# Optimization experiments

Measured on AMD Instinct MI355X. Metric: run time of the kernel, lower is better.

The kernel has to match this reference:

```python
import jax, jax.numpy as jnp
import numpy as np
import math

N = 2048; L = 100; D_IN = 128; D_STATE = 16; D_INNER = 256
MAMBA_DIM = 128; GAT_HID = 64; HEADS = 4; GAT_OUT = 64


def _lin(key, fin, fout, scale=0.02):
    k1, k2 = jax.random.split(key)
    return (jax.random.normal(k1, (fin, fout), jnp.float32) * scale,
            jnp.zeros((fout,), jnp.float32))


def setup_inputs() -> dict:
    key = jax.random.key(0)
    ks = jax.random.split(key, 16)
    temporal_data = jax.random.normal(ks[0], (N, L, D_IN), jnp.float32)
    graph_x = jax.random.normal(ks[1], (N, D_IN), jnp.float32)
    adj = (jax.random.uniform(ks[2], (N, N)) < 0.005).astype(jnp.float32)
    adj_matrix = jnp.maximum(adj, jnp.eye(N, dtype=jnp.float32))
    pos_emb = jax.random.normal(ks[3], (1, 100, D_IN), jnp.float32)
    Wi, bi = _lin(ks[4], D_IN, D_INNER)
    Wg, bg = _lin(ks[5], D_IN, D_INNER)
    A_log = jnp.linspace(math.log(1e-3), math.log(0.1), D_STATE).reshape(1, D_STATE).astype(jnp.float32)
    Wb, bb = _lin(ks[6], D_INNER, D_STATE)
    Wc, bc = _lin(ks[7], D_IN, D_STATE)
    Wo, bo = _lin(ks[8], D_INNER, D_IN)
    Wfc, bfc = _lin(ks[9], D_IN, MAMBA_DIM)
    W1 = jax.random.normal(ks[10], (HEADS, D_IN, GAT_HID), jnp.float32) * 0.05
    a1 = jax.random.normal(ks[11], (HEADS, 2 * GAT_HID), jnp.float32) * 0.05
    W2 = jax.random.normal(ks[12], (1, HEADS * GAT_HID, GAT_OUT), jnp.float32) * 0.05
    a2 = jax.random.normal(ks[13], (1, 2 * GAT_OUT), jnp.float32) * 0.05
    return dict(temporal_data=temporal_data, graph_x=graph_x, adj_matrix=adj_matrix,
                pos_emb=pos_emb, Wi=Wi, bi=bi, Wg=Wg, bg=bg, A_log=A_log,
                Wb=Wb, bb=bb, Wc=Wc, bc=bc, Wo=Wo, bo=bo, Wfc=Wfc, bfc=bfc,
                W1=W1, a1=a1, W2=W2, a2=a2)


def _mamba(x, pos_emb, Wi, bi, Wg, bg, A_log, Wb, bb, Wc, bc, Wo, bo):
    Bt, Ls, _ = x.shape
    x = x + pos_emb[:, :Ls, :]
    x_gated = (x @ Wi + bi) * jax.nn.sigmoid(x @ Wg + bg)   # [B,L,d_inner]
    Bmat = x_gated @ Wb + bb                                 # [B,L,d_state]
    Cmat = x @ Wc + bc                                       # [B,L,d_state]
    A = jnp.exp(0.01 * jnp.exp(A_log))                       # [1,d_state] (dt=0.01)

    def step(h, bc):
        b, c = bc
        h = A * h + b
        return h, h * c

    h0 = jnp.zeros((Bt, A_log.shape[1]), x.dtype)
    _, ys = jax.lax.scan(step, h0, (jnp.swapaxes(Bmat, 0, 1), jnp.swapaxes(Cmat, 0, 1)))
    y = jnp.swapaxes(ys, 0, 1)                               # [B,L,d_state]
    d_inner = Wo.shape[0]
    out_exp = jnp.concatenate(
        [y, jnp.zeros((Bt, Ls, d_inner - y.shape[-1]), x.dtype)], axis=-1)
    return out_exp @ Wo + bo


def _gat_layer(x, adj, W, a, concat):
    # x: [N,Fin], W: [H,Fin,Fout], a: [H,2*Fout]
    F_out = W.shape[2]
    xt = jnp.einsum('nf,hfo->hno', x, W)                     # [H,N,Fout]
    e_src = jnp.einsum('hno,ho->hn', xt, a[:, :F_out])       # a . x_i part
    e_dst = jnp.einsum('hno,ho->hn', xt, a[:, F_out:])       # a . x_j part
    e = jax.nn.leaky_relu(e_src[:, :, None] + e_dst[:, None, :], 0.2)
    e = jnp.where(adj[None, :, :] > 0, e, -jnp.inf)
    att = jax.nn.softmax(e, axis=2)                          # masked entries -> 0
    h_prime = jnp.einsum('hij,hjo->hio', att, xt)            # [H,N,Fout]
    if concat:
        return jnp.transpose(h_prime, (1, 0, 2)).reshape(x.shape[0], -1)
    return h_prime.mean(axis=0)


def reference(temporal_data, graph_x, adj_matrix, pos_emb, Wi, bi, Wg, bg, A_log,
              Wb, bb, Wc, bc, Wo, bo, Wfc, bfc, W1, a1, W2, a2):
    mamba_out = _mamba(temporal_data, pos_emb, Wi, bi, Wg, bg, A_log, Wb, bb, Wc, bc, Wo, bo)
    mamba_features = mamba_out @ Wfc + bfc
    # GAT stack (dropout is identity in eval mode)
    h = _gat_layer(graph_x, adj_matrix, W1, a1, concat=True)
    h = jax.nn.relu(h)
    gat_features = _gat_layer(h, adj_matrix, W2, a2, concat=False)
    return mamba_features, gat_features
```

## Files before the change

kernel.cpp:

```cpp
#include <hip/hip_runtime.h>
#include <hip/hip_bf16.h>

#define N_NODES 2048
#define L_SEQ   100
#define ROWS    (N_NODES * L_SEQ)
#define HEADS   4
#define GHID    64

typedef __attribute__((ext_vector_type(8))) short bf16x8;
typedef __attribute__((ext_vector_type(4))) float floatx4;

__device__ __forceinline__ short f2bf(float f) {
    union { float f; unsigned u; } v; v.f = f;
    return (short)((v.u + 0x8000u) >> 16);
}

constexpr size_t OFF_WCOMB = 0;
constexpr size_t OFF_BCOMB = 2048;
constexpr size_t OFF_AEXP  = 2176;
constexpr size_t OFF_WIGS  = 2192;
constexpr size_t OFF_WBS   = 34960;
constexpr size_t OFF_WCS   = 37008;
constexpr size_t OFF_BM    = 38032;
constexpr size_t OFF_CM    = OFF_BM + (size_t)ROWS * 16;
constexpr size_t OFF_XT1   = OFF_BM;
constexpr size_t OFF_ES1   = OFF_XT1 + (size_t)HEADS * N_NODES * GHID;
constexpr size_t OFF_ED1   = OFF_ES1 + HEADS * N_NODES;
constexpr size_t OFF_H1    = OFF_ED1 + HEADS * N_NODES;
constexpr size_t OFF_XT2   = OFF_H1 + (size_t)N_NODES * 256;
constexpr size_t OFF_ES2   = OFF_XT2 + (size_t)N_NODES * 64;
constexpr size_t OFF_ED2   = OFF_ES2 + N_NODES;

__global__ void k0_comb(const float* __restrict__ Wo, const float* __restrict__ bo,
                        const float* __restrict__ Wfc, const float* __restrict__ bfc,
                        const float* __restrict__ A_log, float* __restrict__ ws) {
    const int b = blockIdx.x, f2 = threadIdx.x;
    if (b < 16) {
        float a = 0.f;
        for (int f = 0; f < 128; f++) a += Wo[b * 128 + f] * Wfc[f * 128 + f2];
        ws[OFF_WCOMB + b * 128 + f2] = a;
    } else {
        float acc = bfc[f2];
        for (int f = 0; f < 128; f++) acc += bo[f] * Wfc[f * 128 + f2];
        ws[OFF_BCOMB + f2] = acc;
        if (f2 < 16) ws[OFF_AEXP + f2] = expf(0.01f * expf(A_log[f2]));
    }
}

__global__ void k0_prep(const float* __restrict__ Wi, const float* __restrict__ Wg,
                        const float* __restrict__ Wb, const float* __restrict__ Wc,
                        float* __restrict__ ws) {
    int i = blockIdx.x * 256 + threadIdx.x;
    short* wigs = (short*)(ws + OFF_WIGS);
    short* wbs  = (short*)(ws + OFF_WBS);
    short* wcs  = (short*)(ws + OFF_WCS);
    if (i < 65536) {
        int j = i & 7, lane = (i >> 3) & 63, ks = (i >> 9) & 3, nt = i >> 11;
        int w = nt >> 3, t = nt & 7;
        int col = w * 64 + (t & 3) * 16 + (lane & 15);
        int k   = ks * 32 + (lane >> 4) * 8 + j;
        float v = (t < 4) ? Wi[k * 256 + col] : Wg[k * 256 + col];
        wigs[i] = f2bf(v);
    } else if (i < 65536 + 4096) {
        int ii = i - 65536;
        int j = ii & 7, lane = (ii >> 3) & 63, ks = ii >> 9;
        int k = ks * 32 + (lane >> 4) * 8 + j, n = lane & 15;
        wbs[ii] = f2bf(Wb[k * 16 + n]);
    } else if (i < 65536 + 4096 + 2048) {
        int ii = i - 65536 - 4096;
        int j = ii & 7, lane = (ii >> 3) & 63, ks = ii >> 9;
        int k = ks * 32 + (lane >> 4) * 8 + j, n = lane & 15;
        wcs[ii] = f2bf(Wc[k * 16 + n]);
    }
}

__global__ __launch_bounds__(256) void k1_mfma(
    const float* __restrict__ temporal, const float* __restrict__ pos,
    const float* __restrict__ bi, const float* __restrict__ bg,
    const float* __restrict__ bb, const float* __restrict__ bc,
    const float* __restrict__ ws, float* __restrict__ Bm, float* __restrict__ Cm) {
    __shared__ short xbf[64][136];
    __shared__ short gbf[64][264];
    const int tid = threadIdx.x, wave = tid >> 6, lane = tid & 63;
    const int m = lane & 15, quad = lane >> 4;
    const int r0 = blockIdx.x * 64;

#pragma unroll
    for (int i = 0; i < 8; i++) {
        int f4  = i * 256 + tid;
        int row = f4 >> 5;
        int c4  = (f4 & 31) * 4;
        int r = r0 + row, l = r % L_SEQ;
        float4 tv = *(const float4*)(temporal + (size_t)r * 128 + c4);
        float4 pv = *(const float4*)(pos + l * 128 + c4);
        short4 sv;
        sv.x = f2bf(tv.x + pv.x); sv.y = f2bf(tv.y + pv.y);
        sv.z = f2bf(tv.z + pv.z); sv.w = f2bf(tv.w + pv.w);
        *(short4*)&xbf[row][c4] = sv;
    }
    __syncthreads();

    const short* Wigs = (const short*)(ws + OFF_WIGS);
    floatx4 acc[4][8] = {};
#pragma unroll
    for (int ks = 0; ks < 4; ks++) {
        bf16x8 bfr[8];
#pragma unroll
        for (int nt = 0; nt < 8; nt++)
            bfr[nt] = *(const bf16x8*)(Wigs + (size_t)(((wave * 8 + nt) * 4 + ks) * 64 + lane) * 8);
        bf16x8 afr[4];
#pragma unroll
        for (int mt = 0; mt < 4; mt++)
            afr[mt] = *(const bf16x8*)&xbf[mt * 16 + m][ks * 32 + quad * 8];
#pragma unroll
        for (int mt = 0; mt < 4; mt++)
#pragma unroll
            for (int nt = 0; nt < 8; nt++)
                acc[mt][nt] = __builtin_amdgcn_mfma_f32_16x16x32_bf16(
                    afr[mt], bfr[nt], acc[mt][nt], 0, 0, 0);
    }

    const float NL2E = -1.44269504f;
#pragma unroll
    for (int tp = 0; tp < 4; tp++) {
        int col = wave * 64 + tp * 16 + m;
        float biv = bi[col];
        float bgs = bg[col] * NL2E;
#pragma unroll
        for (int mt = 0; mt < 4; mt++) {
#pragma unroll
            for (int r = 0; r < 4; r++) {
                float li = acc[mt][tp][r] + biv;
                float ex = __builtin_amdgcn_exp2f(fmaf(acc[mt][tp + 4][r], NL2E, bgs));
                float g  = li * __builtin_amdgcn_rcpf(1.f + ex);
                gbf[mt * 16 + quad * 4 + r][col] = f2bf(g);
            }
        }
    }
    __syncthreads();

    const short* Wbs = (const short*)(ws + OFF_WBS);
    const short* Wcs = (const short*)(ws + OFF_WCS);
    floatx4 accB = {}, accC = {};
#pragma unroll
    for (int ks = 0; ks < 8; ks++) {
        bf16x8 a = *(const bf16x8*)&gbf[wave * 16 + m][ks * 32 + quad * 8];
        bf16x8 b = *(const bf16x8*)(Wbs + (size_t)(ks * 64 + lane) * 8);
        accB = __builtin_amdgcn_mfma_f32_16x16x32_bf16(a, b, accB, 0, 0, 0);
    }
#pragma unroll
    for (int ks = 0; ks < 4; ks++) {
        bf16x8 a = *(const bf16x8*)&xbf[wave * 16 + m][ks * 32 + quad * 8];
        bf16x8 b = *(const bf16x8*)(Wcs + (size_t)(ks * 64 + lane) * 8);
        accC = __builtin_amdgcn_mfma_f32_16x16x32_bf16(a, b, accC, 0, 0, 0);
    }
    float bbv = bb[m], bcv = bc[m];
#pragma unroll
    for (int r = 0; r < 4; r++) {
        int row = r0 + wave * 16 + quad * 4 + r;
        Bm[(size_t)row * 16 + m] = accB[r] + bbv;
        Cm[(size_t)row * 16 + m] = accC[r] + bcv;
    }
}

__global__ __launch_bounds__(128) void k2_scan(const float* __restrict__ ws,
                                               float* __restrict__ out) {
    __shared__ float sb[1600], sc[1600];
    const int n = blockIdx.x, f = threadIdx.x;
    const float4* Bm4 = (const float4*)(ws + OFF_BM + (size_t)n * 1600);
    const float4* Cm4 = (const float4*)(ws + OFF_CM + (size_t)n * 1600);
#pragma unroll
    for (int i = 0; i < 4; i++) {
        int idx = i * 128 + f;
        if (idx < 400) {
            ((float4*)sb)[idx] = Bm4[idx];
            ((float4*)sc)[idx] = Cm4[idx];
        }
    }
    float w[16], A[16], h[16];
#pragma unroll
    for (int s = 0; s < 16; s++) {
        w[s] = ws[OFF_WCOMB + s * 128 + f];
        A[s] = ws[OFF_AEXP + s];
        h[s] = 0.f;
    }
    const float bcb = ws[OFF_BCOMB + f];
    __syncthreads();
    for (int l = 0; l < L_SEQ; l++) {
        float acc = bcb;
#pragma unroll
        for (int s = 0; s < 16; s++) {
            h[s] = A[s] * h[s] + sb[l * 16 + s];
            acc += h[s] * sc[l * 16 + s] * w[s];
        }
        out[((size_t)n * L_SEQ + l) * 128 + f] = acc;
    }
}

__global__ __launch_bounds__(64) void k4_xt1(const float* __restrict__ gx,
                                             const float* __restrict__ W1,
                                             const float* __restrict__ a1,
                                             float* __restrict__ ws) {
    const int b = blockIdx.x;
    const int h = b >> 11;
    const int n = b & 2047;
    const int o = threadIdx.x;
    float acc = 0.f;
    for (int f = 0; f < 128; f++)
        acc += gx[n * 128 + f] * W1[(h * 128 + f) * 64 + o];
    ws[OFF_XT1 + ((size_t)h * 2048 + n) * 64 + o] = acc;
    float es = acc * a1[h * 128 + o];
    float ed = acc * a1[h * 128 + 64 + o];
#pragma unroll
    for (int off = 32; off > 0; off >>= 1) {
        es += __shfl_down(es, off);
        ed += __shfl_down(ed, off);
    }
    if (o == 0) { ws[OFF_ES1 + h * 2048 + n] = es; ws[OFF_ED1 + h * 2048 + n] = ed; }
}

__global__ __launch_bounds__(256) void k5_att1(const float* __restrict__ adj,
                                               const float* __restrict__ ws,
                                               float* __restrict__ h1out) {
    __shared__ int list[2048];
    __shared__ int cnt;
    const int n = blockIdx.x, tid = threadIdx.x;
    if (tid == 0) cnt = 0;
    __syncthreads();
    for (int j = tid; j < 2048; j += 256)
        if (adj[(size_t)n * 2048 + j] > 0.f) list[atomicAdd(&cnt, 1)] = j;
    __syncthreads();
    const int h = tid >> 6, o = tid & 63;
    const float  es = ws[OFF_ES1 + h * 2048 + n];
    const float* ed = ws + OFF_ED1 + h * 2048;
    const float* xt = ws + OFF_XT1 + (size_t)h * 2048 * 64;
    float num = 0.f, den = 0.f;
    const int mm = cnt;
    for (int ii = 0; ii < mm; ii++) {
        int j = list[ii];
        float e = es + ed[j];
        e = (e > 0.f) ? e : 0.2f * e;
        float wgt = expf(e);
        den += wgt;
        num += wgt * xt[(size_t)j * 64 + o];
    }
    float v = num / den;
    h1out[(size_t)n * 256 + h * 64 + o] = v > 0.f ? v : 0.f;
}

__global__ __launch_bounds__(64) void k6_xt2(const float* __restrict__ W2,
                                             const float* __restrict__ a2,
                                             float* __restrict__ ws) {
    const int n = blockIdx.x, o = threadIdx.x;
    const float* h1 = ws + OFF_H1 + (size_t)n * 256;
    float acc = 0.f;
    for (int f = 0; f < 256; f++) acc += h1[f] * W2[f * 64 + o];
    ws[OFF_XT2 + (size_t)n * 64 + o] = acc;
    float es = acc * a2[o];
    float ed = acc * a2[64 + o];
#pragma unroll
    for (int off = 32; off > 0; off >>= 1) {
        es += __shfl_down(es, off);
        ed += __shfl_down(ed, off);
    }
    if (o == 0) { ws[OFF_ES2 + n] = es; ws[OFF_ED2 + n] = ed; }
}

__global__ __launch_bounds__(64) void k7_att2(const float* __restrict__ adj,
                                              const float* __restrict__ ws,
                                              float* __restrict__ gout) {
    __shared__ int list[2048];
    __shared__ int cnt;
    const int n = blockIdx.x, o = threadIdx.x;
    if (o == 0) cnt = 0;
    __syncthreads();
    for (int j = o; j < 2048; j += 64)
        if (adj[(size_t)n * 2048 + j] > 0.f) list[atomicAdd(&cnt, 1)] = j;
    __syncthreads();
    const float es = ws[OFF_ES2 + n];
    float num = 0.f, den = 0.f;
    const int mm = cnt;
    for (int ii = 0; ii < mm; ii++) {
        int j = list[ii];
        float e = es + ws[OFF_ED2 + j];
        e = (e > 0.f) ? e : 0.2f * e;
        float wgt = expf(e);
        den += wgt;
        num += wgt * ws[OFF_XT2 + (size_t)j * 64 + o];
    }
    gout[(size_t)n * 64 + o] = num / den;
}

extern "C" void kernel_launch(void* const* d_in, const int* in_sizes, int n_in,
                              void* d_out, int out_size, void* d_ws, size_t ws_size,
                              hipStream_t stream) {
    const float* temporal = (const float*)d_in[0];
    const float* graph_x  = (const float*)d_in[1];
    const float* adj      = (const float*)d_in[2];
    const float* pos      = (const float*)d_in[3];
    const float* Wi  = (const float*)d_in[4];
    const float* bi  = (const float*)d_in[5];
    const float* Wg  = (const float*)d_in[6];
    const float* bg  = (const float*)d_in[7];
    const float* A_log = (const float*)d_in[8];
    const float* Wb  = (const float*)d_in[9];
    const float* bb  = (const float*)d_in[10];
    const float* Wc  = (const float*)d_in[11];
    const float* bc  = (const float*)d_in[12];
    const float* Wo  = (const float*)d_in[13];
    const float* bo  = (const float*)d_in[14];
    const float* Wfc = (const float*)d_in[15];
    const float* bfc = (const float*)d_in[16];
    const float* W1  = (const float*)d_in[17];
    const float* a1  = (const float*)d_in[18];
    const float* W2  = (const float*)d_in[19];
    const float* a2  = (const float*)d_in[20];

    float* ws = (float*)d_ws;
    float* out_mamba = (float*)d_out;
    float* out_gat   = out_mamba + (size_t)ROWS * 128;

    k0_comb<<<17, 128, 0, stream>>>(Wo, bo, Wfc, bfc, A_log, ws);
    k0_prep<<<280, 256, 0, stream>>>(Wi, Wg, Wb, Wc, ws);
    k1_mfma<<<ROWS / 64, 256, 0, stream>>>(temporal, pos, bi, bg, bb, bc, ws,
                                           ws + OFF_BM, ws + OFF_CM);
    k2_scan<<<N_NODES, 128, 0, stream>>>(ws, out_mamba);
    k4_xt1<<<HEADS * N_NODES, 64, 0, stream>>>(graph_x, W1, a1, ws);
    k5_att1<<<N_NODES, 256, 0, stream>>>(adj, ws, ws + OFF_H1);
    k6_xt2<<<N_NODES, 64, 0, stream>>>(W2, a2, ws);
    k7_att2<<<N_NODES, 64, 0, stream>>>(adj, ws, out_gat);
}
```

Measured before the change: 378.1 us.

## Split k1 work across 8 waves to halve per-wave accumulators

```diff
diff --git a/kernel.cpp b/kernel.cpp
--- a/kernel.cpp
+++ b/kernel.cpp
@@ -74,7 +74,7 @@
     }
 }
 
-__global__ __launch_bounds__(256) void k1_mfma(
+__global__ __launch_bounds__(512, 4) void k1_mfma(
     const float* __restrict__ temporal, const float* __restrict__ pos,
     const float* __restrict__ bi, const float* __restrict__ bg,
     const float* __restrict__ bb, const float* __restrict__ bc,
@@ -84,14 +84,15 @@
     const int tid = threadIdx.x, wave = tid >> 6, lane = tid & 63;
     const int m = lane & 15, quad = lane >> 4;
     const int r0 = blockIdx.x * 64;
-
-#pragma unroll
-    for (int i = 0; i < 8; i++) {
-        int f4  = i * 256 + tid;
+    const int l0 = r0 % L_SEQ;
+
+#pragma unroll
+    for (int i = 0; i < 4; i++) {
+        int f4  = i * 512 + tid;
         int row = f4 >> 5;
         int c4  = (f4 & 31) * 4;
-        int r = r0 + row, l = r % L_SEQ;
-        float4 tv = *(const float4*)(temporal + (size_t)r * 128 + c4);
+        int l = l0 + row; if (l >= L_SEQ) l -= L_SEQ;
+        float4 tv = *(const float4*)(temporal + (size_t)(r0 + row) * 128 + c4);
         float4 pv = *(const float4*)(pos + l * 128 + c4);
         short4 sv;
         sv.x = f2bf(tv.x + pv.x); sv.y = f2bf(tv.y + pv.y);
@@ -101,13 +102,16 @@
     __syncthreads();
 
     const short* Wigs = (const short*)(ws + OFF_WIGS);
-    floatx4 acc[4][8] = {};
+    const int wg = wave >> 1, wp = wave & 1;
+    floatx4 acc[4][4] = {};
 #pragma unroll
     for (int ks = 0; ks < 4; ks++) {
-        bf16x8 bfr[8];
-#pragma unroll
-        for (int nt = 0; nt < 8; nt++)
-            bfr[nt] = *(const bf16x8*)(Wigs + (size_t)(((wave * 8 + nt) * 4 + ks) * 64 + lane) * 8);
+        bf16x8 bfr[4];
+#pragma unroll
+        for (int jl = 0; jl < 4; jl++) {
+            int ntg = wg * 8 + wp * 2 + (jl & 1) + ((jl >> 1) << 2);
+            bfr[jl] = *(const bf16x8*)(Wigs + (size_t)((ntg * 4 + ks) * 64 + lane) * 8);
+        }
         bf16x8 afr[4];
 #pragma unroll
         for (int mt = 0; mt < 4; mt++)
@@ -115,15 +119,15 @@
 #pragma unroll
         for (int mt = 0; mt < 4; mt++)
 #pragma unroll
-            for (int nt = 0; nt < 8; nt++)
-                acc[mt][nt] = __builtin_amdgcn_mfma_f32_16x16x32_bf16(
-                    afr[mt], bfr[nt], acc[mt][nt], 0, 0, 0);
+            for (int jl = 0; jl < 4; jl++)
+                acc[mt][jl] = __builtin_amdgcn_mfma_f32_16x16x32_bf16(
+                    afr[mt], bfr[jl], acc[mt][jl], 0, 0, 0);
     }
 
     const float NL2E = -1.44269504f;
 #pragma unroll
-    for (int tp = 0; tp < 4; tp++) {
-        int col = wave * 64 + tp * 16 + m;
+    for (int tp = 0; tp < 2; tp++) {
+        int col = wave * 32 + tp * 16 + m;
         float biv = bi[col];
         float bgs = bg[col] * NL2E;
 #pragma unroll
@@ -131,7 +135,7 @@
 #pragma unroll
             for (int r = 0; r < 4; r++) {
                 float li = acc[mt][tp][r] + biv;
-                float ex = __builtin_amdgcn_exp2f(fmaf(acc[mt][tp + 4][r], NL2E, bgs));
+                float ex = __builtin_amdgcn_exp2f(fmaf(acc[mt][tp + 2][r], NL2E, bgs));
                 float g  = li * __builtin_amdgcn_rcpf(1.f + ex);
                 gbf[mt * 16 + quad * 4 + r][col] = f2bf(g);
             }
@@ -139,27 +143,37 @@
     }
     __syncthreads();
 
-    const short* Wbs = (const short*)(ws + OFF_WBS);
-    const short* Wcs = (const short*)(ws + OFF_WCS);
-    floatx4 accB = {}, accC = {};
-#pragma unroll
-    for (int ks = 0; ks < 8; ks++) {
-        bf16x8 a = *(const bf16x8*)&gbf[wave * 16 + m][ks * 32 + quad * 8];
-        bf16x8 b = *(const bf16x8*)(Wbs + (size_t)(ks * 64 + lane) * 8);
-        accB = __builtin_amdgcn_mfma_f32_16x16x32_bf16(a, b, accB, 0, 0, 0);
-    }
-#pragma unroll
-    for (int ks = 0; ks < 4; ks++) {
-        bf16x8 a = *(const bf16x8*)&xbf[wave * 16 + m][ks * 32 + quad * 8];
-        bf16x8 b = *(const bf16x8*)(Wcs + (size_t)(ks * 64 + lane) * 8);
-        accC = __builtin_amdgcn_mfma_f32_16x16x32_bf16(a, b, accC, 0, 0, 0);
-    }
-    float bbv = bb[m], bcv = bc[m];
-#pragma unroll
-    for (int r = 0; r < 4; r++) {
-        int row = r0 + wave * 16 + quad * 4 + r;
-        Bm[(size_t)row * 16 + m] = accB[r] + bbv;
-        Cm[(size_t)row * 16 + m] = accC[r] + bcv;
+    if (wave < 4) {
+        const short* Wbs = (const short*)(ws + OFF_WBS);
+        floatx4 accB = {};
+#pragma unroll
+        for (int ks = 0; ks < 8; ks++) {
+            bf16x8 a = *(const bf16x8*)&gbf[wave * 16 + m][ks * 32 + quad * 8];
+            bf16x8 b = *(const bf16x8*)(Wbs + (size_t)(ks * 64 + lane) * 8);
+            accB = __builtin_amdgcn_mfma_f32_16x16x32_bf16(a, b, accB, 0, 0, 0);
+        }
+        float bbv = bb[m];
+#pragma unroll
+        for (int r = 0; r < 4; r++) {
+            int row = r0 + wave * 16 + quad * 4 + r;
+            Bm[(size_t)row * 16 + m] = accB[r] + bbv;
+        }
+    } else {
+        const short* Wcs = (const short*)(ws + OFF_WCS);
+        const int mt = wave - 4;
+        floatx4 accC = {};
+#pragma unroll
+        for (int ks = 0; ks < 4; ks++) {
+            bf16x8 a = *(const bf16x8*)&xbf[mt * 16 + m][ks * 32 + quad * 8];
+            bf16x8 b = *(const bf16x8*)(Wcs + (size_t)(ks * 64 + lane) * 8);
+            accC = __builtin_amdgcn_mfma_f32_16x16x32_bf16(a, b, accC, 0, 0, 0);
+        }
+        float bcv = bc[m];
+#pragma unroll
+        for (int r = 0; r < 4; r++) {
+            int row = r0 + mt * 16 + quad * 4 + r;
+            Cm[(size_t)row * 16 + m] = accC[r] + bcv;
+        }
     }
 }
 
@@ -322,7 +336,7 @@
 
     k0_comb<<<17, 128, 0, stream>>>(Wo, bo, Wfc, bfc, A_log, ws);
     k0_prep<<<280, 256, 0, stream>>>(Wi, Wg, Wb, Wc, ws);
-    k1_mfma<<<ROWS / 64, 256, 0, stream>>>(temporal, pos, bi, bg, bb, bc, ws,
+    k1_mfma<<<ROWS / 64, 512, 0, stream>>>(temporal, pos, bi, bg, bb, bc, ws,
                                            ws + OFF_BM, ws + OFF_CM);
     k2_scan<<<N_NODES, 128, 0, stream>>>(ws, out_mamba);
     k4_xt1<<<HEADS * N_NODES, 64, 0, stream>>>(graph_x, W1, a1, ws);
```

Measured after the change: 353.2 us. 1.07x faster.
